# Optimization experiments

Measured on AMD Instinct MI355X. Metric: run time of the kernel, lower is better.

## Reference

```python
import jax, jax.numpy as jnp
import numpy as np

EPS_NORM = 1e-12   # F.normalize eps
EPS_W = 1e-8       # weight eps in knn


def _l2_normalize(x):
    n = jnp.linalg.norm(x, axis=-1, keepdims=True)
    return x / jnp.maximum(n, EPS_NORM)


def setup_inputs() -> dict:
    key = jax.random.key(0)
    k1, k2, k3 = jax.random.split(key, 3)
    B, N, D, T = 2048, 100000, 128, 8
    return {
        "query": jax.random.normal(k1, (B, D), dtype=jnp.float32),
        "supports": jax.random.normal(k2, (N, D), dtype=jnp.float32),
        "targets": jax.random.uniform(k3, (N, T), dtype=jnp.float32),
        "k": 16,
    }


def reference(query, supports, targets, k):
    q = _l2_normalize(query)           # [B, D]
    s = _l2_normalize(supports)        # [N, D]
    dists = 1.0 - q @ s.T              # [B, N] cosine distance
    k = min(k, dists.shape[-1])
    # smallest-k distances == largest-k of negated distances
    neg_d, idx = jax.lax.top_k(-dists, k)   # [B, k]
    d = -neg_d
    w = 1.0 / (d + EPS_W)
    w = w / jnp.sum(w, axis=-1, keepdims=True)          # [B, k]
    tv = targets[idx]                                    # [B, k, T] gather
    return jnp.sum(tv * w[..., None], axis=1)            # [B, T]
```

## Files before the change

kernel.cpp:

```cpp
#include <hip/hip_runtime.h>


#define NSLICES 64
#define CN 64
#define BQ 128
#define NSUB 100
#define NGS (NSLICES * NSUB)
#define QCAP 64
#define THR_MARGIN 0.013f

typedef __bf16 bf16x8 __attribute__((ext_vector_type(8)));
typedef float f32x4 __attribute__((ext_vector_type(4)));

__device__ __forceinline__ ushort f2bf_rne(float f) {
  unsigned u = __float_as_uint(f);
  return (ushort)((u + 0x7FFFu + ((u >> 16) & 1u)) >> 16);
}
__device__ __forceinline__ ushort f2bf_down(float f) {
  unsigned u = __float_as_uint(f);
  return (ushort)((u >> 16) + (u >> 31));
}
__device__ __forceinline__ unsigned bf2key(ushort b) {
  return (unsigned)(b ^ ((b & 0x8000u) ? 0xFFFFu : 0x8000u));
}

__device__ __forceinline__ void bitonic64(float& v, unsigned& i, int lane) {
  #pragma unroll
  for (int k = 2; k <= 64; k <<= 1) {
    #pragma unroll
    for (int j = k >> 1; j > 0; j >>= 1) {
      float pv = __shfl_xor(v, j);
      unsigned pi = (unsigned)__shfl_xor((int)i, j);
      bool up = ((lane & k) == 0);
      bool lower = ((lane & j) == 0);
      bool gt = (v > pv) || (v == pv && i > pi);
      bool keep = (up == lower) ? !gt : gt;
      if (!keep) { v = pv; i = pi; }
    }
  }
}

__global__ __launch_bounds__(256) void norm_rows_k(
    const float* __restrict__ sup, const float* __restrict__ qry,
    ushort* __restrict__ sb, ushort* __restrict__ qb, int N, int nq) {
  int row = blockIdx.x * 4 + (threadIdx.x >> 6);
  int lane = threadIdx.x & 63;
  if (row >= N + nq) return;
  const float* src = (row < N) ? (sup + (size_t)row * 128)
                               : (qry + (size_t)(row - N) * 128);
  ushort* dst = (row < N) ? (sb + (size_t)row * 128)
                          : (qb + (size_t)(row - N) * 128);
  float2 v = *reinterpret_cast<const float2*>(src + lane * 2);
  float ss = v.x * v.x + v.y * v.y;
  #pragma unroll
  for (int o = 1; o < 64; o <<= 1) ss += __shfl_xor(ss, o);
  float inv = 1.0f / fmaxf(sqrtf(ss), 1e-12f);
  ushort2 h = make_ushort2(f2bf_rne(v.x * inv), f2bf_rne(v.y * inv));
  *reinterpret_cast<ushort2*>(dst + lane * 2) = h;
}

__device__ __forceinline__ void stage_lin(const ushort* __restrict__ sn,
                                          ushort* dst, int cb, int s1, int tid) {
  #pragma unroll
  for (int r = 0; r < 4; ++r) {
    int o = (r << 12) + tid * 16;
    int row = o >> 8;
    int dj = (o >> 4) & 15;
    int sj = dj ^ (row & 7);
    int srow = min(cb + row, s1 - 1);
    __builtin_amdgcn_global_load_lds(
        (const unsigned int*)(sn + (size_t)srow * 128 + sj * 8),
        (unsigned int*)(dst + (o >> 1)), 16, 0, 0);
  }
}

__device__ __forceinline__ void stage_list(const ushort* __restrict__ sn,
                                           ushort* dst, const ushort* slist_b,
                                           int s0, int s1, int tid) {
  #pragma unroll
  for (int r = 0; r < 4; ++r) {
    int o = (r << 12) + tid * 16;
    int row = o >> 8;
    int dj = (o >> 4) & 15;
    int sj = dj ^ (row & 7);
    int sub = slist_b[row >> 4];
    int lrow = (sub == 0xFFFF) ? 0 : sub * 16 + (row & 15);
    int srow = min(s0 + lrow, s1 - 1);
    __builtin_amdgcn_global_load_lds(
        (const unsigned int*)(sn + (size_t)srow * 128 + sj * 8),
        (unsigned int*)(dst + (o >> 1)), 16, 0, 0);
  }
}

__global__ __launch_bounds__(256, 4) void pass1_k(
    const ushort* __restrict__ qn, const ushort* __restrict__ sn,
    ushort* __restrict__ cm, int N) {
  __shared__ ushort st[2][CN * 128];
  const int tid = threadIdx.x;
  const int w = tid >> 6, lane = tid & 63, g = lane >> 4, m = lane & 15;
  const int L = blockIdx.x;
  const int xcd = L & 7, i6 = L >> 3;
  const int qtile = i6 & 15;
  const int slice = (xcd << 3) | (i6 >> 4);
  const int qbase = qtile * BQ;
  const int SLICE = (N + NSLICES - 1) / NSLICES;
  const int s0 = slice * SLICE;
  const int s1 = min(N, s0 + SLICE);
  const int nch = (s1 - s0 + CN - 1) / CN;

  stage_lin(sn, &st[0][0], s0, s1, tid);

  bf16x8 afr[2][4];
  #pragma unroll
  for (int jt = 0; jt < 2; ++jt) {
    int qrow = qbase + w * 32 + jt * 16 + m;
    #pragma unroll
    for (int t = 0; t < 4; ++t)
      afr[jt][t] = *reinterpret_cast<const bf16x8*>(qn + (size_t)qrow * 128 + t * 32 + g * 8);
  }
  __syncthreads();

  int buf = 0;
  for (int ch = 0; ch < nch; ++ch) {
    const int cb = s0 + ch * CN;
    if (ch + 1 < nch) stage_lin(sn, &st[buf ^ 1][0], cb + CN, s1, tid);
    const ushort* stc = &st[buf][0];
    const bool lastch = (ch == nch - 1);
    #pragma unroll
    for (int ct = 0; ct < 4; ++ct) {
      const int srow = ct * 16 + m;
      f32x4 a0 = {0.f, 0.f, 0.f, 0.f}, a1 = {0.f, 0.f, 0.f, 0.f};
      #pragma unroll
      for (int t = 0; t < 4; ++t) {
        int cj = (4 * t + g) ^ (srow & 7);
        bf16x8 sfr = *reinterpret_cast<const bf16x8*>(&stc[srow * 128 + cj * 8]);
        a0 = __builtin_amdgcn_mfma_f32_16x16x32_bf16(sfr, afr[0][t], a0, 0, 0, 0);
        a1 = __builtin_amdgcn_mfma_f32_16x16x32_bf16(sfr, afr[1][t], a1, 0, 0, 0);
      }
      if (lastch) {
        int si = cb + ct * 16 + g * 4;
        #pragma unroll
        for (int e = 0; e < 4; ++e) {
          if (si + e >= s1) { a0[e] = -3.0e38f; a1[e] = -3.0e38f; }
        }
      }
      float v0 = fmaxf(fmaxf(a0[0], a0[1]), fmaxf(a0[2], a0[3]));
      float v1 = fmaxf(fmaxf(a1[0], a1[1]), fmaxf(a1[2], a1[3]));
      v0 = fmaxf(v0, __shfl_xor(v0, 16));
      v0 = fmaxf(v0, __shfl_xor(v0, 32));
      v1 = fmaxf(v1, __shfl_xor(v1, 16));
      v1 = fmaxf(v1, __shfl_xor(v1, 32));
      unsigned u0 = (unsigned)f2bf_down(v0);
      unsigned u1 = (unsigned)f2bf_down(v1);
      unsigned w0 = u0 | ((unsigned)__shfl_xor((int)u0, 1) << 16);
      unsigned w1 = u1 | ((unsigned)__shfl_xor((int)u1, 1) << 16);
      unsigned x0 = (unsigned)__shfl_xor((int)w0, 2);
      unsigned x1 = (unsigned)__shfl_xor((int)w1, 2);
      if (g == 0 && (m & 3) == 0) {
        int gs = slice * NSUB + ch * 4 + ct;
        int q0 = qbase + w * 32 + m;
        int q1 = q0 + 16;
        *reinterpret_cast<uint2*>(cm + ((size_t)(q0 >> 2) * NGS + gs) * 4) =
            make_uint2(w0, x0);
        *reinterpret_cast<uint2*>(cm + ((size_t)(q1 >> 2) * NGS + gs) * 4) =
            make_uint2(w1, x1);
      }
    }
    __syncthreads();
    buf ^= 1;
  }

  const int miss = NSUB - nch * 4;
  for (int idx = tid; idx < miss * BQ; idx += 256) {
    int sub = nch * 4 + idx / BQ;
    int q = qbase + (idx % BQ);
    cm[((size_t)(q >> 2) * NGS + (size_t)(slice * NSUB + sub)) * 4 + (q & 3)] = 0xFF80;
  }
}

__global__ __launch_bounds__(256) void thr_k(const ushort* __restrict__ cm,
                                             float* __restrict__ thr,
                                             unsigned* __restrict__ cnt) {
  const int q = blockIdx.x * 4 + (threadIdx.x >> 6);
  const int lane = threadIdx.x & 63;
  const size_t base = (size_t)(q >> 2) * NGS * 4 + (q & 3);
  unsigned keys[NGS / 128];
  #pragma unroll
  for (int j = 0; j < NGS / 128; ++j) {
    unsigned k0 = bf2key(cm[base + (size_t)(lane + 128 * j) * 4]);
    unsigned k1 = bf2key(cm[base + (size_t)(lane + 64 + 128 * j) * 4]);
    keys[j] = k0 | (k1 << 16);
  }
  unsigned res = 0;
  for (int b = 15; b >= 0; --b) {
    unsigned t = res | (1u << b);
    int c = 0;
    #pragma unroll
    for (int j = 0; j < NGS / 128; ++j)
      c += (int)((keys[j] & 0xFFFFu) >= t) + (int)((keys[j] >> 16) >= t);
    #pragma unroll
    for (int o = 1; o < 64; o <<= 1) c += __shfl_xor(c, o);
    if (c >= 16) res = t;
  }
  if (lane == 0) {
    ushort b16 = (ushort)((res & 0x8000u) ? (res ^ 0x8000u) : (res ^ 0xFFFFu));
    thr[q] = __uint_as_float((unsigned)b16 << 16) - THR_MARGIN;
    cnt[q] = 0;
  }
}

__global__ __launch_bounds__(256, 4) void pass2_k(
    const ushort* __restrict__ qn, const ushort* __restrict__ sn,
    const ushort* __restrict__ cm, const float* __restrict__ thr,
    unsigned* __restrict__ cnt, float2* __restrict__ candq, int N) {
  __shared__ ushort st[2][CN * 128];
  __shared__ float thr_l[BQ];
  __shared__ unsigned char hit[NSUB];
  __shared__ ushort slist[NSUB + 4];
  __shared__ int nhit_s;

  const int tid = threadIdx.x;
  const int w = tid >> 6, lane = tid & 63, g = lane >> 4, m = lane & 15;
  const int L = blockIdx.x;
  const int xcd = L & 7, i6 = L >> 3;
  const int qtile = i6 & 15;
  const int slice = (xcd << 3) | (i6 >> 4);
  const int qbase = qtile * BQ;
  const int SLICE = (N + NSLICES - 1) / NSLICES;
  const int s0 = slice * SLICE;
  const int s1 = min(N, s0 + SLICE);
  const int slen = s1 - s0;

  if (tid < BQ) thr_l[tid] = thr[qbase + tid];
  if (tid < NSUB) hit[tid] = 0;
  __syncthreads();

  {
    int q = qbase + (tid & 127);
    int sh = tid >> 7;
    float tq = thr_l[tid & 127];
    size_t base = (size_t)(q >> 2) * NGS * 4 + (q & 3);
    for (int j = 0; j < NSUB / 2; ++j) {
      int s = 2 * j + sh;
      ushort b = cm[base + (size_t)(slice * NSUB + s) * 4];
      if (__uint_as_float((unsigned)b << 16) >= tq) hit[s] = 1;
    }
  }
  __syncthreads();
  if (tid < 64) {
    int total = 0;
    #pragma unroll
    for (int r = 0; r < 2; ++r) {
      int idx = r * 64 + tid;
      bool f = (idx < NSUB) && hit[idx];
      unsigned long long bm = __ballot(f);
      int pos = total + __popcll(bm & ((1ull << tid) - 1ull));
      if (f) slist[pos] = (ushort)idx;
      total += __popcll(bm);
    }
    if (tid == 0) {
      nhit_s = total;
      #pragma unroll
      for (int p = 0; p < 4; ++p) slist[total + p] = 0xFFFF;
    }
  }
  __syncthreads();
  const int nhit = nhit_s;
  if (nhit == 0) return;
  const int nb = (nhit + 3) >> 2;

  bf16x8 afr[2][4];
  #pragma unroll
  for (int jt = 0; jt < 2; ++jt) {
    int qrow = qbase + w * 32 + jt * 16 + m;
    #pragma unroll
    for (int t = 0; t < 4; ++t)
      afr[jt][t] = *reinterpret_cast<const bf16x8*>(qn + (size_t)qrow * 128 + t * 32 + g * 8);
  }
  const float thrq0 = thr_l[w * 32 + m];
  const float thrq1 = thr_l[w * 32 + 16 + m];

  stage_list(sn, &st[0][0], &slist[0], s0, s1, tid);
  __syncthreads();

  int buf = 0;
  for (int b = 0; b < nb; ++b) {
    if (b + 1 < nb) stage_list(sn, &st[buf ^ 1][0], &slist[(b + 1) * 4], s0, s1, tid);
    const ushort* stc = &st[buf][0];
    #pragma unroll
    for (int ct = 0; ct < 4; ++ct) {
      const int srow = ct * 16 + m;
      f32x4 a0 = {0.f, 0.f, 0.f, 0.f}, a1 = {0.f, 0.f, 0.f, 0.f};
      #pragma unroll
      for (int t = 0; t < 4; ++t) {
        int cj = (4 * t + g) ^ (srow & 7);
        bf16x8 sfr = *reinterpret_cast<const bf16x8*>(&stc[srow * 128 + cj * 8]);
        a0 = __builtin_amdgcn_mfma_f32_16x16x32_bf16(sfr, afr[0][t], a0, 0, 0, 0);
        a1 = __builtin_amdgcn_mfma_f32_16x16x32_bf16(sfr, afr[1][t], a1, 0, 0, 0);
      }
      int sub = slist[b * 4 + ct];
      if (sub != 0xFFFF) {
        int li0 = sub * 16 + g * 4;
        bool h0[4], h1[4];
        bool any = false;
        #pragma unroll
        for (int e = 0; e < 4; ++e) {
          bool ok = (li0 + e) < slen;
          h0[e] = ok && (a0[e] >= thrq0);
          h1[e] = ok && (a1[e] >= thrq1);
          any = any || h0[e] || h1[e];
        }
        if (__any(any)) {
          #pragma unroll
          for (int e = 0; e < 4; ++e) {
            if (h0[e]) {
              int q = qbase + w * 32 + m;
              unsigned p = atomicAdd(&cnt[q], 1u);
              if (p < (unsigned)QCAP)
                candq[(size_t)q * QCAP + p] =
                    make_float2(a0[e], __int_as_float(s0 + li0 + e));
            }
            if (h1[e]) {
              int q = qbase + w * 32 + 16 + m;
              unsigned p = atomicAdd(&cnt[q], 1u);
              if (p < (unsigned)QCAP)
                candq[(size_t)q * QCAP + p] =
                    make_float2(a1[e], __int_as_float(s0 + li0 + e));
            }
          }
        }
      }
    }
    __syncthreads();
    buf ^= 1;
  }
}

__global__ __launch_bounds__(256) void merge_refine_k(
    const float* __restrict__ query, const float* __restrict__ supports,
    const float* __restrict__ targets, const unsigned* __restrict__ cnt,
    const float2* __restrict__ candq, float* __restrict__ out) {
  const int W = threadIdx.x >> 6;
  const int q = blockIdx.x * 4 + W;
  const int lane = threadIdx.x & 63;
  __shared__ float qh_s[4][128];
  __shared__ float2 list[4][QCAP];
  __shared__ float2 refd[4][QCAP];

  int total = min((int)cnt[q], QCAP);
  if (lane < total) list[W][lane] = candq[(size_t)q * QCAP + lane];

  float2 qv = *reinterpret_cast<const float2*>(query + (size_t)q * 128 + lane * 2);
  double qss = (double)qv.x * qv.x + (double)qv.y * qv.y;
  #pragma unroll
  for (int o = 1; o < 64; o <<= 1) qss += __shfl_xor(qss, o);
  float qn1 = fmaxf((float)sqrt(qss), 1e-12f);
  qh_s[W][lane * 2] = qv.x / qn1;
  qh_s[W][lane * 2 + 1] = qv.y / qn1;
  __syncthreads();

  const int g16 = lane >> 4, m16 = lane & 15;
  float qh[8];
  #pragma unroll
  for (int d = 0; d < 8; ++d) qh[d] = qh_s[W][m16 * 8 + d];
  int rounds = (total + 3) >> 2;
  for (int r = 0; r < rounds; ++r) {
    int cc = r * 4 + g16;
    bool valid = cc < total;
    float2 ce = valid ? list[W][cc] : make_float2(0.f, __int_as_float(0));
    int sidx = __float_as_int(ce.y);
    float4 sa = *reinterpret_cast<const float4*>(supports + (size_t)sidx * 128 + m16 * 8);
    float4 sb = *reinterpret_cast<const float4*>(supports + (size_t)sidx * 128 + m16 * 8 + 4);
    float sv[8] = {sa.x, sa.y, sa.z, sa.w, sb.x, sb.y, sb.z, sb.w};
    double ss = 0.0, dt = 0.0;
    #pragma unroll
    for (int d = 0; d < 8; ++d) {
      ss += (double)sv[d] * sv[d];
      dt += (double)qh[d] * sv[d];
    }
    #pragma unroll
    for (int o = 1; o < 16; o <<= 1) {
      ss += __shfl_xor(ss, o);
      dt += __shfl_xor(dt, o);
    }
    if (m16 == 0 && valid) {
      float sn1 = fmaxf((float)sqrt(ss), 1e-12f);
      refd[W][cc] = make_float2((float)(1.0 - dt / (double)sn1), ce.y);
    }
  }
  __syncthreads();

  float dv = (lane < total) ? refd[W][lane].x : 3.0e38f;
  unsigned di = (lane < total) ? (unsigned)__float_as_int(refd[W][lane].y) : 0xFFFFFFFFu;
  bitonic64(dv, di, lane);

  float wv = (lane < 16) ? 1.0f / (dv + 1e-8f) : 0.0f;
  float wsum = wv;
  #pragma unroll
  for (int o = 1; o < 64; o <<= 1) wsum += __shfl_xor(wsum, o);
  float acc[8];
  #pragma unroll
  for (int t = 0; t < 8; ++t) acc[t] = 0.f;
  if (lane < 16) {
    float wn = wv / wsum;
    const float* tp = targets + (size_t)di * 8;
    #pragma unroll
    for (int t = 0; t < 8; ++t) acc[t] = wn * tp[t];
  }
  #pragma unroll
  for (int o = 1; o < 16; o <<= 1) {
    #pragma unroll
    for (int t = 0; t < 8; ++t) acc[t] += __shfl_xor(acc[t], o);
  }
  if (lane == 0) {
    #pragma unroll
    for (int t = 0; t < 8; ++t) out[(size_t)q * 8 + t] = acc[t];
  }
}

extern "C" void kernel_launch(void* const* d_in, const int* in_sizes, int n_in,
                              void* d_out, int out_size, void* d_ws, size_t ws_size,
                              hipStream_t stream) {
  const float* query = (const float*)d_in[0];
  const float* supports = (const float*)d_in[1];
  const float* targets = (const float*)d_in[2];
  float* out = (float*)d_out;
  const int D = 128;
  const int B = in_sizes[0] / D;
  const int N = in_sizes[1] / D;

  char* ws = (char*)d_ws;
  size_t off = 0;
  ushort* sn = (ushort*)(ws + off); off += (size_t)N * D * 2;
  off = (off + 255) & ~(size_t)255;
  ushort* qn = (ushort*)(ws + off); off += (size_t)B * D * 2;
  off = (off + 255) & ~(size_t)255;
  ushort* cm = (ushort*)(ws + off); off += (size_t)B * NGS * 2;
  off = (off + 255) & ~(size_t)255;
  float* thr = (float*)(ws + off); off += (size_t)B * 4;
  off = (off + 255) & ~(size_t)255;
  unsigned* cnt = (unsigned*)(ws + off); off += (size_t)B * 4;
  off = (off + 255) & ~(size_t)255;
  float2* candq = (float2*)(ws + off); off += (size_t)B * QCAP * sizeof(float2);
  if (off > ws_size) return;

  hipLaunchKernelGGL(norm_rows_k, dim3((N + B + 3) / 4), dim3(256), 0, stream,
                     supports, query, sn, qn, N, B);
  int nblk = (B / BQ) * NSLICES;
  hipLaunchKernelGGL(pass1_k, dim3(nblk), dim3(256), 0, stream, qn, sn, cm, N);
  hipLaunchKernelGGL(thr_k, dim3(B / 4), dim3(256), 0, stream, cm, thr, cnt);
  hipLaunchKernelGGL(pass2_k, dim3(nblk), dim3(256), 0, stream, qn, sn, cm, thr, cnt, candq, N);
  hipLaunchKernelGGL(merge_refine_k, dim3(B / 4), dim3(256), 0, stream, query, supports, targets, cnt, candq, out);
}
```

Before: 188.2 us.

## Switch distance GEMMs to 32x32x16 MFMA with 32-row subgroups

Result: faster. 174.2 us (-7.4%).

```diff
diff --git a/kernel.cpp b/kernel.cpp
--- a/kernel.cpp
+++ b/kernel.cpp
@@ -4,13 +4,13 @@
 #define NSLICES 64
 #define CN 64
 #define BQ 128
-#define NSUB 100
+#define NSUB 50
 #define NGS (NSLICES * NSUB)
 #define QCAP 64
 #define THR_MARGIN 0.013f
 
 typedef __bf16 bf16x8 __attribute__((ext_vector_type(8)));
-typedef float f32x4 __attribute__((ext_vector_type(4)));
+typedef float f32x16 __attribute__((ext_vector_type(16)));
 
 __device__ __forceinline__ ushort f2bf_rne(float f) {
   unsigned u = __float_as_uint(f);
@@ -66,7 +66,7 @@
     int o = (r << 12) + tid * 16;
     int row = o >> 8;
     int dj = (o >> 4) & 15;
-    int sj = dj ^ (row & 7);
+    int sj = dj ^ (row & 15);
     int srow = min(cb + row, s1 - 1);
     __builtin_amdgcn_global_load_lds(
         (const unsigned int*)(sn + (size_t)srow * 128 + sj * 8),
@@ -82,9 +82,9 @@
     int o = (r << 12) + tid * 16;
     int row = o >> 8;
     int dj = (o >> 4) & 15;
-    int sj = dj ^ (row & 7);
-    int sub = slist_b[row >> 4];
-    int lrow = (sub == 0xFFFF) ? 0 : sub * 16 + (row & 15);
+    int sj = dj ^ (row & 15);
+    int sub = slist_b[row >> 5];
+    int lrow = (sub == 0xFFFF) ? 0 : sub * 32 + (row & 31);
     int srow = min(s0 + lrow, s1 - 1);
     __builtin_amdgcn_global_load_lds(
         (const unsigned int*)(sn + (size_t)srow * 128 + sj * 8),
@@ -97,7 +97,8 @@
     ushort* __restrict__ cm, int N) {
   __shared__ ushort st[2][CN * 128];
   const int tid = threadIdx.x;
-  const int w = tid >> 6, lane = tid & 63, g = lane >> 4, m = lane & 15;
+  const int w = tid >> 6, lane = tid & 63;
+  const int q32 = lane & 31, half = lane >> 5;
   const int L = blockIdx.x;
   const int xcd = L & 7, i6 = L >> 3;
   const int qtile = i6 & 15;
@@ -110,13 +111,12 @@
 
   stage_lin(sn, &st[0][0], s0, s1, tid);
 
-  bf16x8 afr[2][4];
-  #pragma unroll
-  for (int jt = 0; jt < 2; ++jt) {
-    int qrow = qbase + w * 32 + jt * 16 + m;
-    #pragma unroll
-    for (int t = 0; t < 4; ++t)
-      afr[jt][t] = *reinterpret_cast<const bf16x8*>(qn + (size_t)qrow * 128 + t * 32 + g * 8);
+  bf16x8 afr[8];
+  {
+    const int qrow = qbase + w * 32 + q32;
+    #pragma unroll
+    for (int t = 0; t < 8; ++t)
+      afr[t] = *reinterpret_cast<const bf16x8*>(qn + (size_t)qrow * 128 + t * 16 + half * 8);
   }
   __syncthreads();
 
@@ -126,53 +126,51 @@
     if (ch + 1 < nch) stage_lin(sn, &st[buf ^ 1][0], cb + CN, s1, tid);
     const ushort* stc = &st[buf][0];
     const bool lastch = (ch == nch - 1);
-    #pragma unroll
-    for (int ct = 0; ct < 4; ++ct) {
-      const int srow = ct * 16 + m;
-      f32x4 a0 = {0.f, 0.f, 0.f, 0.f}, a1 = {0.f, 0.f, 0.f, 0.f};
+
+    f32x16 a0 = {0.f}, a1 = {0.f};
+    #pragma unroll
+    for (int r = 1; r < 16; ++r) { a0[r] = 0.f; a1[r] = 0.f; }
+    const int r0 = q32;
+    #pragma unroll
+    for (int t = 0; t < 8; ++t) {
+      int jb = t * 2 + half;
+      int cj0 = jb ^ (r0 & 15);
+      int cj1 = jb ^ ((r0 + 32) & 15);
+      bf16x8 s0 = *reinterpret_cast<const bf16x8*>(&stc[r0 * 128 + cj0 * 8]);
+      bf16x8 s1 = *reinterpret_cast<const bf16x8*>(&stc[(r0 + 32) * 128 + cj1 * 8]);
+      a0 = __builtin_amdgcn_mfma_f32_32x32x16_bf16(s0, afr[t], a0, 0, 0, 0);
+      a1 = __builtin_amdgcn_mfma_f32_32x32x16_bf16(s1, afr[t], a1, 0, 0, 0);
+    }
+    float v0 = -3.0e38f, v1 = -3.0e38f;
+    if (lastch) {
       #pragma unroll
-      for (int t = 0; t < 4; ++t) {
-        int cj = (4 * t + g) ^ (srow & 7);
-        bf16x8 sfr = *reinterpret_cast<const bf16x8*>(&stc[srow * 128 + cj * 8]);
-        a0 = __builtin_amdgcn_mfma_f32_16x16x32_bf16(sfr, afr[0][t], a0, 0, 0, 0);
-        a1 = __builtin_amdgcn_mfma_f32_16x16x32_bf16(sfr, afr[1][t], a1, 0, 0, 0);
-      }
-      if (lastch) {
-        int si = cb + ct * 16 + g * 4;
-        #pragma unroll
-        for (int e = 0; e < 4; ++e) {
-          if (si + e >= s1) { a0[e] = -3.0e38f; a1[e] = -3.0e38f; }
-        }
-      }
-      float v0 = fmaxf(fmaxf(a0[0], a0[1]), fmaxf(a0[2], a0[3]));
-      float v1 = fmaxf(fmaxf(a1[0], a1[1]), fmaxf(a1[2], a1[3]));
-      v0 = fmaxf(v0, __shfl_xor(v0, 16));
-      v0 = fmaxf(v0, __shfl_xor(v0, 32));
-      v1 = fmaxf(v1, __shfl_xor(v1, 16));
-      v1 = fmaxf(v1, __shfl_xor(v1, 32));
-      unsigned u0 = (unsigned)f2bf_down(v0);
-      unsigned u1 = (unsigned)f2bf_down(v1);
-      unsigned w0 = u0 | ((unsigned)__shfl_xor((int)u0, 1) << 16);
-      unsigned w1 = u1 | ((unsigned)__shfl_xor((int)u1, 1) << 16);
-      unsigned x0 = (unsigned)__shfl_xor((int)w0, 2);
-      unsigned x1 = (unsigned)__shfl_xor((int)w1, 2);
-      if (g == 0 && (m & 3) == 0) {
-        int gs = slice * NSUB + ch * 4 + ct;
-        int q0 = qbase + w * 32 + m;
-        int q1 = q0 + 16;
-        *reinterpret_cast<uint2*>(cm + ((size_t)(q0 >> 2) * NGS + gs) * 4) =
-            make_uint2(w0, x0);
-        *reinterpret_cast<uint2*>(cm + ((size_t)(q1 >> 2) * NGS + gs) * 4) =
-            make_uint2(w1, x1);
-      }
+      for (int r = 0; r < 16; ++r) {
+        int row = (r & 3) + 8 * (r >> 2) + (half << 2);
+        if (cb + row < s1) v0 = fmaxf(v0, a0[r]);
+        if (cb + 32 + row < s1) v1 = fmaxf(v1, a1[r]);
+      }
+    } else {
+      #pragma unroll
+      for (int r = 0; r < 16; ++r) {
+        v0 = fmaxf(v0, a0[r]);
+        v1 = fmaxf(v1, a1[r]);
+      }
+    }
+    v0 = fmaxf(v0, __shfl_xor(v0, 32));
+    v1 = fmaxf(v1, __shfl_xor(v1, 32));
+    if (lane < 32) {
+      int q = qbase + w * 32 + q32;
+      size_t e0 = ((size_t)(q >> 2) * NGS + slice * NSUB + ch * 2) * 4 + (q & 3);
+      cm[e0] = f2bf_down(v0);
+      cm[e0 + 4] = f2bf_down(v1);
     }
     __syncthreads();
     buf ^= 1;
   }
 
-  const int miss = NSUB - nch * 4;
+  const int miss = NSUB - nch * 2;
   for (int idx = tid; idx < miss * BQ; idx += 256) {
-    int sub = nch * 4 + idx / BQ;
+    int sub = nch * 2 + idx / BQ;
     int q = qbase + (idx % BQ);
     cm[((size_t)(q >> 2) * NGS + (size_t)(slice * NSUB + sub)) * 4 + (q & 3)] = 0xFF80;
   }
@@ -216,11 +214,12 @@
   __shared__ ushort st[2][CN * 128];
   __shared__ float thr_l[BQ];
   __shared__ unsigned char hit[NSUB];
-  __shared__ ushort slist[NSUB + 4];
+  __shared__ ushort slist[NSUB + 2];
   __shared__ int nhit_s;
 
   const int tid = threadIdx.x;
-  const int w = tid >> 6, lane = tid & 63, g = lane >> 4, m = lane & 15;
+  const int w = tid >> 6, lane = tid & 63;
+  const int q32 = lane & 31, half = lane >> 5;
   const int L = blockIdx.x;
   const int xcd = L & 7, i6 = L >> 3;
   const int qtile = i6 & 15;
@@ -248,85 +247,90 @@
   }
   __syncthreads();
   if (tid < 64) {
-    int total = 0;
-    #pragma unroll
-    for (int r = 0; r < 2; ++r) {
-      int idx = r * 64 + tid;
-      bool f = (idx < NSUB) && hit[idx];
-      unsigned long long bm = __ballot(f);
-      int pos = total + __popcll(bm & ((1ull << tid) - 1ull));
-      if (f) slist[pos] = (ushort)idx;
-      total += __popcll(bm);
-    }
+    bool f = (tid < NSUB) && hit[tid];
+    unsigned long long bm = __ballot(f);
+    int pos = __popcll(bm & ((1ull << tid) - 1ull));
+    if (f) slist[pos] = (ushort)tid;
     if (tid == 0) {
+      int total = __popcll(bm);
       nhit_s = total;
-      #pragma unroll
-      for (int p = 0; p < 4; ++p) slist[total + p] = 0xFFFF;
+      slist[total] = 0xFFFF;
+      slist[total + 1] = 0xFFFF;
     }
   }
   __syncthreads();
   const int nhit = nhit_s;
   if (nhit == 0) return;
-  const int nb = (nhit + 3) >> 2;
-
-  bf16x8 afr[2][4];
-  #pragma unroll
-  for (int jt = 0; jt < 2; ++jt) {
-    int qrow = qbase + w * 32 + jt * 16 + m;
-    #pragma unroll
-    for (int t = 0; t < 4; ++t)
-      afr[jt][t] = *reinterpret_cast<const bf16x8*>(qn + (size_t)qrow * 128 + t * 32 + g * 8);
-  }
-  const float thrq0 = thr_l[w * 32 + m];
-  const float thrq1 = thr_l[w * 32 + 16 + m];
+  const int nb = (nhit + 1) >> 1;
+
+  bf16x8 afr[8];
+  {
+    const int qrow = qbase + w * 32 + q32;
+    #pragma unroll
+    for (int t = 0; t < 8; ++t)
+      afr[t] = *reinterpret_cast<const bf16x8*>(qn + (size_t)qrow * 128 + t * 16 + half * 8);
+  }
+  const float thrq = thr_l[w * 32 + q32];
 
   stage_list(sn, &st[0][0], &slist[0], s0, s1, tid);
   __syncthreads();
 
   int buf = 0;
   for (int b = 0; b < nb; ++b) {
-    if (b + 1 < nb) stage_list(sn, &st[buf ^ 1][0], &slist[(b + 1) * 4], s0, s1, tid);
+    if (b + 1 < nb) stage_list(sn, &st[buf ^ 1][0], &slist[(b + 1) * 2], s0, s1, tid);
     const ushort* stc = &st[buf][0];
-    #pragma unroll
-    for (int ct = 0; ct < 4; ++ct) {
-      const int srow = ct * 16 + m;
-      f32x4 a0 = {0.f, 0.f, 0.f, 0.f}, a1 = {0.f, 0.f, 0.f, 0.f};
+
+    f32x16 a0 = {0.f}, a1 = {0.f};
+    #pragma unroll
+    for (int r = 1; r < 16; ++r) { a0[r] = 0.f; a1[r] = 0.f; }
+    const int r0 = q32;
+    #pragma unroll
+    for (int t = 0; t < 8; ++t) {
+      int jb = t * 2 + half;
+      int cj = jb ^ (r0 & 15);
+      bf16x8 sf0 = *reinterpret_cast<const bf16x8*>(&stc[r0 * 128 + cj * 8]);
+      bf16x8 sf1 = *reinterpret_cast<const bf16x8*>(&stc[(r0 + 32) * 128 + cj * 8]);
+      a0 = __builtin_amdgcn_mfma_f32_32x32x16_bf16(sf0, afr[t], a0, 0, 0, 0);
+      a1 = __builtin_amdgcn_mfma_f32_32x32x16_bf16(sf1, afr[t], a1, 0, 0, 0);
+    }
+    const int subA = slist[b * 2], subB = slist[b * 2 + 1];
+    const int q = qbase + w * 32 + q32;
+    if (subA != 0xFFFF) {
+      unsigned hm = 0;
       #pragma unroll
-      for (int t = 0; t < 4; ++t) {
-        int cj = (4 * t + g) ^ (srow & 7);
-        bf16x8 sfr = *reinterpret_cast<const bf16x8*>(&stc[srow * 128 + cj * 8]);
-        a0 = __builtin_amdgcn_mfma_f32_16x16x32_bf16(sfr, afr[0][t], a0, 0, 0, 0);
-        a1 = __builtin_amdgcn_mfma_f32_16x16x32_bf16(sfr, afr[1][t], a1, 0, 0, 0);
-      }
-      int sub = slist[b * 4 + ct];
-      if (sub != 0xFFFF) {
-        int li0 = sub * 16 + g * 4;
-        bool h0[4], h1[4];
-        bool any = false;
+      for (int r = 0; r < 16; ++r) {
+        int row = (r & 3) + 8 * (r >> 2) + (half << 2);
+        if (subA * 32 + row < slen && a0[r] >= thrq) hm |= 1u << r;
+      }
+      if (__any(hm != 0u)) {
         #pragma unroll
-        for (int e = 0; e < 4; ++e) {
-          bool ok = (li0 + e) < slen;
-          h0[e] = ok && (a0[e] >= thrq0);
-          h1[e] = ok && (a1[e] >= thrq1);
-          any = any || h0[e] || h1[e];
+        for (int r = 0; r < 16; ++r) {
+          if (hm & (1u << r)) {
+            int row = (r & 3) + 8 * (r >> 2) + (half << 2);
+            unsigned p = atomicAdd(&cnt[q], 1u);
+            if (p < (unsigned)QCAP)
+              candq[(size_t)q * QCAP + p] =
+                  make_float2(a0[r], __int_as_float(s0 + subA * 32 + row));
+          }
         }
-        if (__any(any)) {
-          #pragma unroll
-          for (int e = 0; e < 4; ++e) {
-            if (h0[e]) {
-              int q = qbase + w * 32 + m;
-              unsigned p = atomicAdd(&cnt[q], 1u);
-              if (p < (unsigned)QCAP)
-                candq[(size_t)q * QCAP + p] =
-                    make_float2(a0[e], __int_as_float(s0 + li0 + e));
-            }
-            if (h1[e]) {
-              int q = qbase + w * 32 + 16 + m;
-              unsigned p = atomicAdd(&cnt[q], 1u);
-              if (p < (unsigned)QCAP)
-                candq[(size_t)q * QCAP + p] =
-                    make_float2(a1[e], __int_as_float(s0 + li0 + e));
-            }
+      }
+    }
+    if (subB != 0xFFFF) {
+      unsigned hm = 0;
+      #pragma unroll
+      for (int r = 0; r < 16; ++r) {
+        int row = (r & 3) + 8 * (r >> 2) + (half << 2);
+        if (subB * 32 + row < slen && a1[r] >= thrq) hm |= 1u << r;
+      }
+      if (__any(hm != 0u)) {
+        #pragma unroll
+        for (int r = 0; r < 16; ++r) {
+          if (hm & (1u << r)) {
+            int row = (r & 3) + 8 * (r >> 2) + (half << 2);
+            unsigned p = atomicAdd(&cnt[q], 1u);
+            if (p < (unsigned)QCAP)
+              candq[(size_t)q * QCAP + p] =
+                  make_float2(a1[r], __int_as_float(s0 + subB * 32 + row));
           }
         }
       }
```
